# Optimization experiments

Hardware: AMD Instinct MI355X
Metric: run time of the kernel (lower is better)

Reference implementation:

```python
import jax, jax.numpy as jnp
import numpy as np

SEM_ENC_DIM = 1024
SENT_HIDDEN_DIM = 1024
ATT_DIM = 512

def setup_inputs() -> dict:
    key = jax.random.key(0)
    ks = jax.random.split(key, 8)
    B, L = 64, 2048
    s = lambda d: 1.0 / np.sqrt(d)
    return {
        "sem_enc_output": jax.random.normal(ks[0], (B, L, SEM_ENC_DIM), dtype=jnp.float32),
        "dec_hidden_state": jax.random.normal(ks[1], (B, SENT_HIDDEN_DIM), dtype=jnp.float32),
        "W_enc": jax.random.uniform(ks[2], (SEM_ENC_DIM, ATT_DIM), jnp.float32, -s(SEM_ENC_DIM), s(SEM_ENC_DIM)),
        "b_enc": jax.random.uniform(ks[3], (ATT_DIM,), jnp.float32, -s(SEM_ENC_DIM), s(SEM_ENC_DIM)),
        "W_dec": jax.random.uniform(ks[4], (SENT_HIDDEN_DIM, ATT_DIM), jnp.float32, -s(SENT_HIDDEN_DIM), s(SENT_HIDDEN_DIM)),
        "b_dec": jax.random.uniform(ks[5], (ATT_DIM,), jnp.float32, -s(SENT_HIDDEN_DIM), s(SENT_HIDDEN_DIM)),
        "W_full": jax.random.uniform(ks[6], (ATT_DIM, 1), jnp.float32, -s(ATT_DIM), s(ATT_DIM)),
        "b_full": jax.random.uniform(ks[7], (1,), jnp.float32, -s(ATT_DIM), s(ATT_DIM)),
    }

def reference(sem_enc_output, dec_hidden_state, W_enc, b_enc, W_dec, b_dec, W_full, b_full):
    # enc projection: [B, L, att_dim]
    enc_proj = jnp.einsum('ble,ea->bla', sem_enc_output, W_enc) + b_enc
    # dec projection: [B, att_dim]
    dec_proj = dec_hidden_state @ W_dec + b_dec
    # broadcast add + tanh: [B, L, att_dim]
    joined = jnp.tanh(enc_proj + dec_proj[:, None, :])
    # scoring: [B, L]
    scores = (jnp.einsum('bla,a->bl', joined, W_full[:, 0]) + b_full[0])
    att_scores = jax.nn.softmax(scores, axis=1)
    # weighted sum over L of the PROJECTED encoder output (matches torch code)
    att_output = jnp.einsum('bl,bla->ba', att_scores, enc_proj)
    return (att_output, att_scores)
```

## Files before the change

### kernel.cpp

```cpp
#include <hip/hip_runtime.h>
#include <hip/hip_bf16.h>
#include <cstdint>
#include <cstddef>

#define BB   64
#define LL   2048
#define ED   1024
#define AD   512
#define BM   128
#define BK   32
#define NCH  (LL / BM)
#define KST  (ED / BK)

typedef short  short8  __attribute__((ext_vector_type(8)));
typedef float  f32x4   __attribute__((ext_vector_type(4)));

__device__ __forceinline__ unsigned short f2bf(float x) {
  unsigned u = __float_as_uint(x);
  u += 0x7FFFu + ((u >> 16) & 1u);
  return (unsigned short)(u >> 16);
}

#define GLOAD_LDS16(gp, lp)                                                        \
  __builtin_amdgcn_global_load_lds(                                                \
      (const __attribute__((address_space(1))) unsigned int*)(gp),                 \
      (__attribute__((address_space(3))) unsigned int*)(lp), 16, 0, 0)

__global__ __launch_bounds__(512) void prep_kernel(
    const float* __restrict__ W_enc, const float* __restrict__ dec,
    const float* __restrict__ W_dec, const float* __restrict__ b_dec,
    unsigned short* __restrict__ Wb, float* __restrict__ dp) {
  const int blk = blockIdx.x, t = threadIdx.x;
  if (blk < BB) {
    const float* drow = dec + blk * ED;
    float a0 = 0.f, a1 = 0.f, a2 = 0.f, a3 = 0.f;
    for (int k = 0; k < ED; k += 4) {
      a0 = fmaf(drow[k],     W_dec[(k)     * AD + t], a0);
      a1 = fmaf(drow[k + 1], W_dec[(k + 1) * AD + t], a1);
      a2 = fmaf(drow[k + 2], W_dec[(k + 2) * AD + t], a2);
      a3 = fmaf(drow[k + 3], W_dec[(k + 3) * AD + t], a3);
    }
    dp[blk * AD + t] = (a0 + a1) + (a2 + a3) + b_dec[t];
  } else {
    const int base = (blk - BB) * 4096;
#pragma unroll
    for (int i = 0; i < 8; i++) {
      const int idx = base + i * 512 + t;
      const int k = idx >> 9, n = idx & 511;
      Wb[((k >> 3) * AD + n) * 8 + (k & 7)] = f2bf(W_enc[idx]);
    }
  }
}

__global__ __launch_bounds__(512, 2) void fused_kernel(
    const float* __restrict__ sem, const unsigned short* __restrict__ Wb,
    const float* __restrict__ dp, const float* __restrict__ b_enc,
    const float* __restrict__ Wf,
    float* __restrict__ raw_scores,
    float* __restrict__ ws_ms, float* __restrict__ ws_o) {

  __shared__ unsigned short Alds[2][4096];
  __shared__ unsigned short Blds[2][16384];

  const int t    = threadIdx.x;
  const int lane = t & 63;
  const int wave = t >> 6;
  const int wm   = wave >> 2;
  const int wn   = wave & 3;
  const int b    = blockIdx.y;
  const int chunk= blockIdx.x;
  const int l0   = chunk * BM;

  const int srow = t >> 2;
  const int skg  = t & 3;
  const float* aptr = sem + ((size_t)(b * LL + l0 + srow)) * ED + skg * 8;
  const unsigned short* bsrc = Wb + t * 8;
  const int awr = skg * 1024 + srow * 8;

  const int arow  = lane & 15;
  const int akg   = lane >> 4;
  const int abase = akg * 1024 + (wm * 64 + arow) * 8;
  const int bbase = akg * 4096 + (wn * 128 + arow) * 8;

  f32x4 acc[4][8];
#pragma unroll
  for (int i = 0; i < 4; i++)
#pragma unroll
    for (int j = 0; j < 8; j++) acc[i][j] = (f32x4)0.f;

  f32x4 pA0 = *(const f32x4*)(aptr);
  f32x4 pA1 = *(const f32x4*)(aptr + 4);
  f32x4 qA0 = *(const f32x4*)(aptr + BK);
  f32x4 qA1 = *(const f32x4*)(aptr + BK + 4);
#pragma unroll
  for (int i = 0; i < 4; i++)
    GLOAD_LDS16(bsrc + i * 4096, &Blds[0][t * 8 + i * 4096]);
  {
    short8 aw;
    aw[0]=(short)f2bf(pA0[0]); aw[1]=(short)f2bf(pA0[1]); aw[2]=(short)f2bf(pA0[2]); aw[3]=(short)f2bf(pA0[3]);
    aw[4]=(short)f2bf(pA1[0]); aw[5]=(short)f2bf(pA1[1]); aw[6]=(short)f2bf(pA1[2]); aw[7]=(short)f2bf(pA1[3]);
    *(short8*)&Alds[0][awr] = aw;
  }
  __syncthreads();

#define ITER(ks, CA0, CA1, LA0, LA1)                                              \
  {                                                                               \
    const int cb = (ks) & 1, nb = ((ks) + 1) & 1;                                 \
    if ((ks) + 1 < KST) {                                                         \
      short8 aw;                                                                  \
      aw[0]=(short)f2bf(CA0[0]); aw[1]=(short)f2bf(CA0[1]);                       \
      aw[2]=(short)f2bf(CA0[2]); aw[3]=(short)f2bf(CA0[3]);                       \
      aw[4]=(short)f2bf(CA1[0]); aw[5]=(short)f2bf(CA1[1]);                       \
      aw[6]=(short)f2bf(CA1[2]); aw[7]=(short)f2bf(CA1[3]);                       \
      *(short8*)&Alds[nb][awr] = aw;                                              \
    }                                                                             \
    if ((ks) + 2 < KST) {                                                         \
      const float* ap = aptr + ((ks) + 2) * BK;                                   \
      LA0 = *(const f32x4*)(ap);                                                  \
      LA1 = *(const f32x4*)(ap + 4);                                              \
    }                                                                             \
    if ((ks) + 1 < KST) {                                                         \
      const unsigned short* bs = bsrc + ((ks) + 1) * 16384;                       \
      _Pragma("unroll")                                                           \
      for (int i = 0; i < 4; i++)                                                 \
        GLOAD_LDS16(bs + i * 4096, &Blds[nb][t * 8 + i * 4096]);                  \
    }                                                                             \
    short8 av[4], bv[8];                                                          \
    _Pragma("unroll")                                                             \
    for (int mf = 0; mf < 4; mf++)                                                \
      av[mf] = *(const short8*)&Alds[cb][abase + mf * 128];                       \
    _Pragma("unroll")                                                             \
    for (int nf = 0; nf < 8; nf++)                                                \
      bv[nf] = *(const short8*)&Blds[cb][bbase + nf * 128];                       \
    _Pragma("unroll")                                                             \
    for (int mf = 0; mf < 4; mf++)                                                \
      _Pragma("unroll")                                                           \
      for (int nf = 0; nf < 8; nf++)                                              \
        acc[mf][nf] = __builtin_amdgcn_mfma_f32_16x16x32_bf16(av[mf], bv[nf], acc[mf][nf], 0, 0, 0); \
    __syncthreads();                                                              \
  }

  for (int kk = 0; kk < KST; kk += 2) {
    ITER(kk,     qA0, qA1, pA0, pA1);
    ITER(kk + 1, pA0, pA1, qA0, qA1);
  }
#undef ITER

  float* eb = (float*)&Blds[0][0];
  float (*sc_part)[4]   = (float (*)[4])eb;
  float* scores_lds     = eb + 512;
  float* weight         = eb + 640;
  float (*o_lds)[AD]    = (float (*)[AD])(eb + 768);
  float* bcv            = eb + 1792;

  float dpv[8], wfv[8], bev[8];
#pragma unroll
  for (int nf = 0; nf < 8; nf++) {
    const int c = wn * 128 + nf * 16 + arow;
    dpv[nf] = dp[b * AD + c];
    wfv[nf] = Wf[c];
    bev[nf] = b_enc[c];
  }
#pragma unroll
  for (int mf = 0; mf < 4; mf++) {
#pragma unroll
    for (int r = 0; r < 4; r++) {
      float p = 0.f;
#pragma unroll
      for (int nf = 0; nf < 8; nf++) {
        float e = acc[mf][nf][r] + bev[nf];
        acc[mf][nf][r] = e;
        float x = e + dpv[nf];
        float ex = __expf(2.f * x);
        float th = 1.f - 2.f / (ex + 1.f);
        p = fmaf(th, wfv[nf], p);
      }
      p += __shfl_xor(p, 1); p += __shfl_xor(p, 2);
      p += __shfl_xor(p, 4); p += __shfl_xor(p, 8);
      if (arow == 0) sc_part[wm * 64 + mf * 16 + akg * 4 + r][wn] = p;
    }
  }
  __syncthreads();

  if (t < BM) {
    float s = sc_part[t][0] + sc_part[t][1] + sc_part[t][2] + sc_part[t][3];
    scores_lds[t] = s;
    raw_scores[(size_t)b * LL + l0 + t] = s;
  }
  __syncthreads();
  if (t < 64) {
    float m = fmaxf(scores_lds[t], scores_lds[t + 64]);
#pragma unroll
    for (int off = 1; off < 64; off <<= 1) m = fmaxf(m, __shfl_xor(m, off));
    if (t == 0) bcv[0] = m;
  }
  __syncthreads();
  const float m_c = bcv[0];
  if (t < BM) weight[t] = __expf(scores_lds[t] - m_c);
  __syncthreads();
  if (t < 64) {
    float s = weight[t] + weight[t + 64];
#pragma unroll
    for (int off = 1; off < 64; off <<= 1) s += __shfl_xor(s, off);
    if (t == 0) bcv[1] = s;
  }

  float wv[4][4];
#pragma unroll
  for (int mf = 0; mf < 4; mf++)
#pragma unroll
    for (int r = 0; r < 4; r++) wv[mf][r] = weight[wm * 64 + mf * 16 + akg * 4 + r];
#pragma unroll
  for (int nf = 0; nf < 8; nf++) {
    float cp = 0.f;
#pragma unroll
    for (int mf = 0; mf < 4; mf++)
#pragma unroll
      for (int r = 0; r < 4; r++) cp = fmaf(wv[mf][r], acc[mf][nf][r], cp);
    cp += __shfl_xor(cp, 16);
    cp += __shfl_xor(cp, 32);
    if (lane < 16) o_lds[wm][wn * 128 + nf * 16 + lane] = cp;
  }
  __syncthreads();
  if (t < AD)
    ws_o[((size_t)b * NCH + chunk) * AD + t] = o_lds[0][t] + o_lds[1][t];
  if (t == 0) {
    ws_ms[(b * NCH + chunk) * 2]     = m_c;
    ws_ms[(b * NCH + chunk) * 2 + 1] = bcv[1];
  }
}

__global__ __launch_bounds__(256) void finalize_kernel(
    const float* __restrict__ ws_ms, const float* __restrict__ ws_o,
    float* __restrict__ out0, float* __restrict__ outS) {
  const int b = blockIdx.x, t = threadIdx.x;
  float ms[NCH], ss[NCH];
  float M = -1e30f;
#pragma unroll
  for (int i = 0; i < NCH; i++) {
    ms[i] = ws_ms[(b * NCH + i) * 2];
    ss[i] = ws_ms[(b * NCH + i) * 2 + 1];
    M = fmaxf(M, ms[i]);
  }
  float S = 0.f, w[NCH];
#pragma unroll
  for (int i = 0; i < NCH; i++) { w[i] = __expf(ms[i] - M); S = fmaf(ss[i], w[i], S); }
  const float invS = 1.f / S;
  for (int c = t; c < AD; c += 256) {
    float a = 0.f;
#pragma unroll
    for (int i = 0; i < NCH; i++) a = fmaf(ws_o[((size_t)b * NCH + i) * AD + c], w[i], a);
    out0[b * AD + c] = a * invS;
  }
  for (int l = t; l < LL; l += 256) {
    float r = outS[(size_t)b * LL + l];
    outS[(size_t)b * LL + l] = __expf(r - M) * invS;
  }
}

extern "C" void kernel_launch(void* const* d_in, const int* in_sizes, int n_in,
                              void* d_out, int out_size, void* d_ws, size_t ws_size,
                              hipStream_t stream) {
  const float* sem    = (const float*)d_in[0];
  const float* dec    = (const float*)d_in[1];
  const float* W_enc  = (const float*)d_in[2];
  const float* b_enc  = (const float*)d_in[3];
  const float* W_dec  = (const float*)d_in[4];
  const float* b_dec  = (const float*)d_in[5];
  const float* W_full = (const float*)d_in[6];

  float* out0 = (float*)d_out;
  float* outS = out0 + BB * AD;

  char* ws = (char*)d_ws;
  unsigned short* Wb = (unsigned short*)ws;
  float* dpw   = (float*)(ws + (1 << 20));
  float* ws_ms = (float*)(ws + (1 << 20) + (128 << 10));
  float* ws_o  = (float*)(ws + (1 << 20) + (128 << 10) + (8 << 10));

  prep_kernel<<<BB + 128, 512, 0, stream>>>(W_enc, dec, W_dec, b_dec, Wb, dpw);
  dim3 g1(NCH, BB);
  fused_kernel<<<g1, 512, 0, stream>>>(sem, Wb, dpw, b_enc, W_full, outS, ws_ms, ws_o);
  finalize_kernel<<<BB, 256, 0, stream>>>(ws_ms, ws_o, out0, outS);
}
```

Baseline: 287.1 us.

## Pre-swizzle W_enc into fragment order and relax barriers in bf16 GEMM loop

The prep kernel now writes the bf16 W_enc copy directly in MFMA-fragment order, and the A tile is stored to LDS in a matching fragment-major layout. Each lane can then read contiguous 16-byte chunks, which is meant to cut LDS bank conflicts and simplify address math. The B global-to-LDS loads are issued earlier in each iteration, and the full __syncthreads is replaced by a partial vmcnt wait plus s_barrier so that prefetches stay in flight. s_setprio is raised around the MFMA block. The hand-written waitcnt counts depend on the exact order in which loads are issued, so a miscounted wait could cause a race.

```diff
diff --git a/kernel.cpp b/kernel.cpp
--- a/kernel.cpp
+++ b/kernel.cpp
@@ -44,10 +44,16 @@
   } else {
     const int base = (blk - BB) * 4096;
 #pragma unroll
-    for (int i = 0; i < 8; i++) {
-      const int idx = base + i * 512 + t;
-      const int k = idx >> 9, n = idx & 511;
-      Wb[((k >> 3) * AD + n) * 8 + (k & 7)] = f2bf(W_enc[idx]);
+    for (int ii = 0; ii < 8; ii++) {
+      const int o  = base + ii * 512 + t;
+      const int ks = o >> 14;
+      const int i  = (o >> 12) & 3;
+      const int w  = (o >> 9) & 7;
+      const int l  = (o >> 3) & 63;
+      const int j  = o & 7;
+      const int k  = ks * 32 + ((l >> 4) << 3) + j;
+      const int c  = ((i * 8 + w) << 4) + (l & 15);
+      Wb[o] = f2bf(W_enc[k * AD + c]);
     }
   }
 }
@@ -75,12 +81,12 @@
   const int skg  = t & 3;
   const float* aptr = sem + ((size_t)(b * LL + l0 + srow)) * ED + skg * 8;
   const unsigned short* bsrc = Wb + t * 8;
-  const int awr = skg * 1024 + srow * 8;
-
-  const int arow  = lane & 15;
-  const int akg   = lane >> 4;
-  const int abase = akg * 1024 + (wm * 64 + arow) * 8;
-  const int bbase = akg * 4096 + (wn * 128 + arow) * 8;
+  const int awr = (srow >> 4) * 512 + skg * 128 + (srow & 15) * 8;
+
+  const int arow = lane & 15;
+  const int akg  = lane >> 4;
+  const int afr  = wm * 4 * 512 + lane * 8;
+  const int bfr  = wn * 8 * 512 + lane * 8;
 
   f32x4 acc[4][8];
 #pragma unroll
@@ -88,24 +94,33 @@
 #pragma unroll
     for (int j = 0; j < 8; j++) acc[i][j] = (f32x4)0.f;
 
+#pragma unroll
+  for (int i = 0; i < 4; i++)
+    GLOAD_LDS16(bsrc + i * 4096, &Blds[0][i * 4096 + t * 8]);
   f32x4 pA0 = *(const f32x4*)(aptr);
   f32x4 pA1 = *(const f32x4*)(aptr + 4);
   f32x4 qA0 = *(const f32x4*)(aptr + BK);
   f32x4 qA1 = *(const f32x4*)(aptr + BK + 4);
-#pragma unroll
-  for (int i = 0; i < 4; i++)
-    GLOAD_LDS16(bsrc + i * 4096, &Blds[0][t * 8 + i * 4096]);
   {
     short8 aw;
     aw[0]=(short)f2bf(pA0[0]); aw[1]=(short)f2bf(pA0[1]); aw[2]=(short)f2bf(pA0[2]); aw[3]=(short)f2bf(pA0[3]);
     aw[4]=(short)f2bf(pA1[0]); aw[5]=(short)f2bf(pA1[1]); aw[6]=(short)f2bf(pA1[2]); aw[7]=(short)f2bf(pA1[3]);
     *(short8*)&Alds[0][awr] = aw;
   }
-  __syncthreads();
+  asm volatile("s_waitcnt vmcnt(2) lgkmcnt(0)" ::: "memory");
+  __builtin_amdgcn_sched_barrier(0);
+  __builtin_amdgcn_s_barrier();
 
 #define ITER(ks, CA0, CA1, LA0, LA1)                                              \
   {                                                                               \
     const int cb = (ks) & 1, nb = ((ks) + 1) & 1;                                 \
+    if ((ks) + 1 < KST) {                      \
+      const unsigned short* bs = bsrc + ((ks) + 1) * 16384;                       \
+      _Pragma("unroll")                                                           \
+      for (int i = 0; i < 4; i++)                                                 \
+        GLOAD_LDS16(bs + i * 4096, &Blds[nb][i * 4096 + t * 8]);                  \
+    }                                                                             \
+    __builtin_amdgcn_sched_barrier(0);      \
     if ((ks) + 1 < KST) {                                                         \
       short8 aw;                                                                  \
       aw[0]=(short)f2bf(CA0[0]); aw[1]=(short)f2bf(CA0[1]);                       \
@@ -119,25 +134,27 @@
       LA0 = *(const f32x4*)(ap);                                                  \
       LA1 = *(const f32x4*)(ap + 4);                                              \
     }                                                                             \
-    if ((ks) + 1 < KST) {                                                         \
-      const unsigned short* bs = bsrc + ((ks) + 1) * 16384;                       \
-      _Pragma("unroll")                                                           \
-      for (int i = 0; i < 4; i++)                                                 \
-        GLOAD_LDS16(bs + i * 4096, &Blds[nb][t * 8 + i * 4096]);                  \
-    }                                                                             \
     short8 av[4], bv[8];                                                          \
     _Pragma("unroll")                                                             \
     for (int mf = 0; mf < 4; mf++)                                                \
-      av[mf] = *(const short8*)&Alds[cb][abase + mf * 128];                       \
+      av[mf] = *(const short8*)&Alds[cb][afr + mf * 512];                         \
     _Pragma("unroll")                                                             \
     for (int nf = 0; nf < 8; nf++)                                                \
-      bv[nf] = *(const short8*)&Blds[cb][bbase + nf * 128];                       \
+      bv[nf] = *(const short8*)&Blds[cb][bfr + nf * 512];                         \
+    __builtin_amdgcn_s_setprio(1);                                                \
     _Pragma("unroll")                                                             \
     for (int mf = 0; mf < 4; mf++)                                                \
       _Pragma("unroll")                                                           \
       for (int nf = 0; nf < 8; nf++)                                              \
         acc[mf][nf] = __builtin_amdgcn_mfma_f32_16x16x32_bf16(av[mf], bv[nf], acc[mf][nf], 0, 0, 0); \
-    __syncthreads();                                                              \
+    __builtin_amdgcn_s_setprio(0);                                                \
+    if ((ks) + 2 < KST) {                 \
+      asm volatile("s_waitcnt vmcnt(2) lgkmcnt(0)" ::: "memory");                 \
+    } else {                                                                      \
+      asm volatile("s_waitcnt vmcnt(0) lgkmcnt(0)" ::: "memory");                 \
+    }                                                                             \
+    __builtin_amdgcn_sched_barrier(0);                                            \
+    __builtin_amdgcn_s_barrier();                                                 \
   }
 
   for (int kk = 0; kk < KST; kk += 2) {
```

New measurement: 292.0 us. Within noise of the previous version (+1.7%).
